# Kernel optimization log

Hardware: AMD Instinct MI355X
Metric: run time of the kernel (lower is better)

Reference implementation:

```python
import jax, jax.numpy as jnp
import numpy as np

L, D, F, T, V = 12, 1024, 4096, 128, 50257
RESCALE, TAU, EPS = 6, 2.0, 1e-5

# spikingjelly LIFNode spike: heaviside forward, ATan surrogate (alpha=2) backward
@jax.custom_vjp
def _heaviside(x):
    return (x >= 0.0).astype(x.dtype)

def _h_fwd(x):
    return (x >= 0.0).astype(x.dtype), x

def _h_bwd(x, g):
    return (g / (1.0 + (jnp.pi * x) ** 2),)

_heaviside.defvjp(_h_fwd, _h_bwd)


def _ln(x, w, b):
    m = jnp.mean(x)
    v = jnp.mean((x - m) ** 2)
    return (x - m) * jax.lax.rsqrt(v + EPS) * w + b


def _lif(v, x):
    # LIFNode(tau=2, v_threshold=1, v_reset=0, decay_input=True), single step
    v = v + (x - v) / TAU
    s = _heaviside(v - 1.0)
    return v * (1.0 - s), s  # hard reset, binary spike out


def _forward(tokens, emb, pos_emb, ln0_w, ln0_b, ln1_w, ln1_b, ln2_w, ln2_b,
             att_tmk, att_tmv, att_tmr, time_first, time_decay_raw,
             att_kw, att_vw, att_rw, att_ow, ffn_tmk, ffn_tmr,
             ffn_kw, ffn_vw, ffn_rw, lnout_w, lnout_b, head):
    td = -jnp.exp(time_decay_raw)  # load-time transform: time_decay = -exp(w)
    params = (ln1_w, ln1_b, ln2_w, ln2_b, att_tmk, att_tmv, att_tmr,
              time_first, td, att_kw, att_vw, att_rw, att_ow,
              ffn_tmk, ffn_tmr, ffn_kw, ffn_vw, ffn_rw)
    idx = jnp.arange(L)

    def layer_step(x, xs):
        i, p, st = xs
        (l1w, l1b, l2w, l2b, tmk, tmv, tmr, tf, tdec,
         kw, vw, rw, ow, ftmk, ftmr, fkw, fvw, frw) = p
        sx_ff, sx_att, aa, bb, pp, v1, v2 = st
        # ---- SA: time-mixing with exp-weighted state (aa, bb, pp) ----
        xa = _ln(x, l1w, l1b)
        xk = xa * tmk + sx_att * (1.0 - tmk)
        xv = xa * tmv + sx_att * (1.0 - tmv)
        xr = xa * tmr + sx_att * (1.0 - tmr)
        r = jax.nn.sigmoid(rw @ xr)
        k = kw @ xk
        v = vw @ xv
        ww = tf + k
        q = jnp.maximum(pp, ww)
        e1, e2 = jnp.exp(pp - q), jnp.exp(ww - q)
        a = e1 * aa + e2 * v
        b = e1 * bb + e2
        ww2 = pp + tdec
        q2 = jnp.maximum(ww2, k)
        e1, e2 = jnp.exp(ww2 - q2), jnp.exp(k - q2)
        aa_n = e1 * aa + e2 * v
        bb_n = e1 * bb + e2
        v1_n, sa_out = _lif(v1, ow @ (r * (a / b)))
        x = x + sa_out
        # ---- FF: channel mixing ----
        xf = _ln(x, l2w, l2b)
        fxk = xf * ftmk + sx_ff * (1.0 - ftmk)
        fxr = xf * ftmr + sx_ff * (1.0 - ftmr)
        fr = jax.nn.sigmoid(frw @ fxr)
        fk = jnp.square(jax.nn.relu(fkw @ fxk))
        v2_n, ff_out = _lif(v2, fr * (fvw @ fk))
        x = x + ff_out
        x = jnp.where((i + 1) % RESCALE == 0, x * 0.5, x)  # rwkv_rescale
        return x, (xf, xa, aa_n, bb_n, q2, v1_n, v2_n)

    def token_step(st, inp):
        tok, pe = inp
        x = emb[tok] + pe
        x = _ln(x, ln0_w, ln0_b)  # ln0 applied only at layer 0
        x, st_n = jax.lax.scan(layer_step, x, (idx, params, st))
        x = _ln(x, lnout_w, lnout_b)
        return st_n, head @ x

    zz = jnp.zeros((L, D), jnp.float32)
    st0 = (zz, zz, zz, zz, jnp.full((L, D), -1e30, jnp.float32), zz, zz)
    _, logits = jax.lax.scan(token_step, st0, (tokens, pos_emb))
    return logits  # [T, V]


def setup_inputs() -> dict:
    key = jax.random.key(0)
    ks = jax.random.split(key, 20)
    n = lambda k, s, sc: jax.random.normal(k, s, jnp.float32) * sc
    u = lambda k, s: jax.random.uniform(k, s, jnp.float32)
    return {
        "tokens": jax.random.randint(ks[0], (T,), 0, V, dtype=jnp.int32),
        "emb": n(ks[1], (V, D), 0.02),
        "pos_emb": n(ks[2], (T, D), 0.02),
        "ln0_w": jnp.ones((D,), jnp.float32), "ln0_b": jnp.zeros((D,), jnp.float32),
        "ln1_w": jnp.ones((L, D), jnp.float32), "ln1_b": jnp.zeros((L, D), jnp.float32),
        "ln2_w": jnp.ones((L, D), jnp.float32), "ln2_b": jnp.zeros((L, D), jnp.float32),
        "att_tmk": u(ks[3], (L, D)), "att_tmv": u(ks[4], (L, D)), "att_tmr": u(ks[5], (L, D)),
        "time_first": n(ks[6], (L, D), 0.5),
        "time_decay_raw": n(ks[7], (L, D), 0.5),
        "att_kw": n(ks[8], (L, D, D), 0.02), "att_vw": n(ks[9], (L, D, D), 0.02),
        "att_rw": n(ks[10], (L, D, D), 0.02), "att_ow": n(ks[11], (L, D, D), 0.02),
        "ffn_tmk": u(ks[12], (L, D)), "ffn_tmr": u(ks[13], (L, D)),
        "ffn_kw": n(ks[14], (L, F, D), 0.02), "ffn_vw": n(ks[15], (L, D, F), 0.02),
        "ffn_rw": n(ks[16], (L, D, D), 0.02),
        "lnout_w": jnp.ones((D,), jnp.float32), "lnout_b": jnp.zeros((D,), jnp.float32),
        "head": n(ks[17], (V, D), 0.02),
    }


def reference(tokens, emb, pos_emb, ln0_w, ln0_b, ln1_w, ln1_b, ln2_w, ln2_b,
              att_tmk, att_tmv, att_tmr, time_first, time_decay_raw,
              att_kw, att_vw, att_rw, att_ow, ffn_tmk, ffn_tmr,
              ffn_kw, ffn_vw, ffn_rw, lnout_w, lnout_b, head):
    return _forward(tokens, emb, pos_emb, ln0_w, ln0_b, ln1_w, ln1_b, ln2_w, ln2_b,
                    att_tmk, att_tmv, att_tmr, time_first, time_decay_raw,
                    att_kw, att_vw, att_rw, att_ow, ffn_tmk, ffn_tmr,
                    ffn_kw, ffn_vw, ffn_rw, lnout_w, lnout_b, head)
```

## Files before the change

### kernel.cpp

```cpp
#include <hip/hip_runtime.h>
#include <hip/hip_bf16.h>
#include <hip/hip_fp8.h>

#define LL   12
#define DD   1024
#define FF   4096
#define TTOK 128
#define VV   50257
#define NBLK 512
#define NTH  512
#define NGRP 12
#define GBLK 42
#define NHEAD (NBLK - NGRP * GBLK)
#define NSTEP (TTOK / 2 + NGRP)
#define WSC  256.0f
#define XSC  (1.0f / 256.0f)

__device__ __forceinline__ float cld(const float* p) {
    return __hip_atomic_load((float*)p, __ATOMIC_RELAXED, __HIP_MEMORY_SCOPE_AGENT);
}
__device__ __forceinline__ void cst(float* p, float v) {
    __hip_atomic_store(p, v, __ATOMIC_RELAXED, __HIP_MEMORY_SCOPE_AGENT);
}

__device__ __host__ __forceinline__ unsigned short f2bf(float f) {
    union { float f; unsigned u; } x; x.f = f;
    unsigned r = x.u + 0x7fffu + ((x.u >> 16) & 1u);
    return (unsigned short)(r >> 16);
}

__device__ __forceinline__ unsigned pack_bf2(float a, float b) {
    return (unsigned)f2bf(a) | ((unsigned)f2bf(b) << 16);
}

__device__ __forceinline__ void ld8(const float* p, float* o) {
    float4 a = ((const float4*)p)[0], b = ((const float4*)p)[1];
    o[0]=a.x; o[1]=a.y; o[2]=a.z; o[3]=a.w; o[4]=b.x; o[5]=b.y; o[6]=b.z; o[7]=b.w;
}

__device__ __forceinline__ void bf8unpack(uint4 u, float* o) {
    union { unsigned u; float f; } t;
    t.u = u.x << 16;         o[0] = t.f;
    t.u = u.x & 0xffff0000u; o[1] = t.f;
    t.u = u.y << 16;         o[2] = t.f;
    t.u = u.y & 0xffff0000u; o[3] = t.f;
    t.u = u.z << 16;         o[4] = t.f;
    t.u = u.z & 0xffff0000u; o[5] = t.f;
    t.u = u.w << 16;         o[6] = t.f;
    t.u = u.w & 0xffff0000u; o[7] = t.f;
}

__device__ __forceinline__ void xld8(const unsigned short* x, int chunk, float* o) {
    uint4 u = *reinterpret_cast<const uint4*>(x + (chunk << 3));
    bf8unpack(u, o);
}
__device__ __forceinline__ void xres(const unsigned short* xb, int lane, float* o) {
    xld8(xb, lane, o); xld8(xb, lane + 64, o + 8);
}

typedef __attribute__((ext_vector_type(2))) float f32x2_t;

__device__ __forceinline__ void fp8x4(unsigned v, float* o) {
#if __has_builtin(__builtin_amdgcn_cvt_pk_f32_fp8)
    f32x2_t a = __builtin_amdgcn_cvt_pk_f32_fp8(v, false);
    f32x2_t b = __builtin_amdgcn_cvt_pk_f32_fp8(v, true);
    o[0] = a[0]; o[1] = a[1]; o[2] = b[0]; o[3] = b[1];
#else
    #pragma unroll
    for (int i = 0; i < 4; ++i) {
        __hip_fp8_e4m3 t; t.__x = (__hip_fp8_storage_t)((v >> (8 * i)) & 0xffu);
        o[i] = (float)t;
    }
#endif
}

__device__ __forceinline__ unsigned enc_fp8x4(float4 f) {
#if __has_builtin(__builtin_amdgcn_cvt_pk_fp8_f32)
    int d = 0;
    d = __builtin_amdgcn_cvt_pk_fp8_f32(f.x, f.y, d, false);
    d = __builtin_amdgcn_cvt_pk_fp8_f32(f.z, f.w, d, true);
    return (unsigned)d;
#else
    __hip_fp8_e4m3 a(f.x), b(f.y), c(f.z), e(f.w);
    return (unsigned)a.__x | ((unsigned)b.__x << 8) |
           ((unsigned)c.__x << 16) | ((unsigned)e.__x << 24);
#endif
}

__device__ __forceinline__ float dot16u(uint4 w, const float* x) {
    float wf[4], s;
    fp8x4(w.x, wf); s  = wf[0]*x[0] +wf[1]*x[1] +wf[2]*x[2] +wf[3]*x[3];
    fp8x4(w.y, wf); s += wf[0]*x[4] +wf[1]*x[5] +wf[2]*x[6] +wf[3]*x[7];
    fp8x4(w.z, wf); s += wf[0]*x[8] +wf[1]*x[9] +wf[2]*x[10]+wf[3]*x[11];
    fp8x4(w.w, wf); s += wf[0]*x[12]+wf[1]*x[13]+wf[2]*x[14]+wf[3]*x[15];
    return s;
}
__device__ __forceinline__ float dot16f(const float* w, const float* x) {
    float s = 0.f;
    #pragma unroll
    for (int i = 0; i < 16; ++i) s += w[i] * x[i];
    return s;
}

template<bool F8> struct WSeg;
template<> struct WSeg<true>  { uint4 v; };
template<> struct WSeg<false> { float f[16]; };

__device__ __forceinline__ void wseg_load(WSeg<true>& d, const void* w, long row,
                                          int segs, int m, int lane) {
    d.v = *(const uint4*)((const unsigned char*)w + (((row * segs + m) << 10) + (lane << 4)));
}
__device__ __forceinline__ void wseg_load(WSeg<false>& d, const void* w, long row,
                                          int segs, int m, int lane) {
    const float* p = (const float*)w + ((long)(row * segs + m) << 10);
    ld8(p + (lane << 3), d.f);
    ld8(p + 512 + (lane << 3), d.f + 8);
}
__device__ __forceinline__ float wseg_dot(const WSeg<true>& d, const float* x) { return dot16u(d.v, x); }
__device__ __forceinline__ float wseg_dot(const WSeg<false>& d, const float* x) { return dot16f(d.f, x); }

__device__ __forceinline__ float wred(float s) {
    #pragma unroll
    for (int o = 32; o; o >>= 1) s += __shfl_xor(s, o, 64);
    return s;
}

__device__ __forceinline__ void bstats(const float* x, float* red, float& m, float& rs) {
    int tid = threadIdx.x;
    float a = x[tid], b = x[tid + 512];
    float s0 = a + b, s1 = a*a + b*b;
    #pragma unroll
    for (int o = 32; o; o >>= 1) { s0 += __shfl_xor(s0, o, 64); s1 += __shfl_xor(s1, o, 64); }
    if ((tid & 63) == 0) { red[(tid >> 6) * 2] = s0; red[(tid >> 6) * 2 + 1] = s1; }
    __syncthreads();
    float ms = 0.f, qs = 0.f;
    #pragma unroll
    for (int w = 0; w < 8; ++w) { ms += red[w * 2]; qs += red[w * 2 + 1]; }
    ms *= (1.f / 1024.f); qs *= (1.f / 1024.f);
    m = ms; rs = rsqrtf(qs - ms * ms + 1e-5f);
    __syncthreads();
}

__device__ __forceinline__ void grpbar(unsigned* bar, int grp, unsigned n, unsigned& sen) {
    __syncthreads();
    if (threadIdx.x == 0) {
        unsigned s = sen ^ 1u;
        unsigned* cnt = &bar[grp * 64];
        unsigned* sns = &bar[grp * 64 + 32];
        unsigned prev = __hip_atomic_fetch_add(cnt, 1u, __ATOMIC_RELAXED, __HIP_MEMORY_SCOPE_AGENT);
        if (prev == n - 1u) {
            __hip_atomic_store(cnt, 0u, __ATOMIC_RELAXED, __HIP_MEMORY_SCOPE_AGENT);
            asm volatile("s_waitcnt vmcnt(0)" ::: "memory");
            __hip_atomic_store(sns, s, __ATOMIC_RELAXED, __HIP_MEMORY_SCOPE_AGENT);
        } else {
            while (__hip_atomic_load(sns, __ATOMIC_RELAXED, __HIP_MEMORY_SCOPE_AGENT) != s)
                __builtin_amdgcn_s_sleep(1);
        }
    }
    sen ^= 1u;
    __syncthreads();
}

__device__ __forceinline__ void fpub(unsigned* f, unsigned v) {
    __hip_atomic_store(f, v, __ATOMIC_RELAXED, __HIP_MEMORY_SCOPE_AGENT);
}
__device__ __forceinline__ void fwait(unsigned* f, unsigned v) {
    while (__hip_atomic_load(f, __ATOMIC_RELAXED, __HIP_MEMORY_SCOPE_AGENT) < v)
        __builtin_amdgcn_s_sleep(1);
}

struct SP {
    const int* tok; const float* emb; const float* pos;
    const float *l0w, *l0b, *l1w, *l1b, *l2w, *l2b;
    const float *tmk, *tmv, *tmr, *tf, *tdr;
    const float *ftmk, *ftmr, *low, *lob;
    const void *kw, *vw, *rw, *ow, *fkw, *fvw, *frw;
    float *xg, *xmid, *rwkv, *fk, *td;
    float *aa, *bb, *pp, *sxa, *sxf, *v1, *v2;
    float* XbT;
    unsigned* bar;
};

template<bool F8>
__global__ __launch_bounds__(NTH, 4) void spike_wave(SP P) {
    const void* kw  = P.kw;
    const void* vw  = P.vw;
    const void* rw  = P.rw;
    const void* ow  = P.ow;
    const void* fkw = P.fkw;
    const void* fvw = P.fvw;
    const void* frw = P.frw;
    constexpr float XS = F8 ? XSC : 1.0f;

    __shared__ float xl[2][DD];
    __shared__ float xs1[DD];
    __shared__ __align__(16) unsigned short xkb[2][DD], xvb[2][DD], xrb[2][DD];
    __shared__ __align__(16) unsigned short fklb[2][FF];
    __shared__ float red[16];
    __shared__ float kres[2][32], vres[2][32], rres[2][32];
    __shared__ float frl2[2][32];

    const int tid  = threadIdx.x;
    const int b    = blockIdx.x;
    const int wid  = tid >> 6;
    const int lane = tid & 63;
    const bool isHead = (b >= NGRP * GBLK);
    const int grp = isHead ? NGRP : (b / GBLK);
    const int gi  = isHead ? (b - NGRP * GBLK) : (b % GBLK);
    const unsigned gn = isHead ? (unsigned)NHEAD : (unsigned)GBLK;
    int c_beg = 0, c_end = 0, r_beg = 0, r_end = 0;
    if (!isHead) {
        c_beg = (gi * DD) / GBLK; c_end = ((gi + 1) * DD) / GBLK;
        r_beg = (gi * FF) / GBLK; r_end = ((gi + 1) * FF) / GBLK;
    }
    const int nch = c_end - c_beg;
    const int  ld = (isHead ? 0 : grp) * DD;
    const long rw0 = (long)(grp * 2) * DD;
    const long fk0 = (long)(grp * 2) * FF;

    unsigned* done = P.bar + 1024;
    unsigned* rda  = P.bar + 2048;

    auto mat2 = [&](const void* wm, const unsigned short* xb, float* o0, float* o1) {
        float x0r[16], x1r[16];
        xres(xb, lane, x0r);
        xres(xb + DD, lane, x1r);
        for (int c0 = c_beg + (wid << 2); c0 < c_end; c0 += 32) {
            WSeg<F8> w[4];
            #pragma unroll
            for (int k = 0; k < 4; ++k) {
                int c = c0 + k;
                wseg_load(w[k], wm, (long)ld + (c < c_end ? c : c0), 1, 0, lane);
            }
            #pragma unroll
            for (int k = 0; k < 4; ++k) {
                float d0 = wred(wseg_dot(w[k], x0r));
                float d1 = wred(wseg_dot(w[k], x1r));
                if (lane == 0 && c0 + k < c_end) {
                    o0[c0 + k - c_beg] = d0; o1[c0 + k - c_beg] = d1;
                }
            }
        }
    };

    unsigned sen = 0;

    if (!isHead) {
        for (int c = c_beg + tid; c < c_end; c += NTH) {
            int si = ld + c;
            P.aa[si] = 0.f; P.bb[si] = 0.f; P.pp[si] = -1e30f;
            P.v1[si] = 0.f; P.v2[si] = 0.f;
            P.td[si] = -expf(P.tdr[si]);
            cst(&P.sxa[si], 0.f); cst(&P.sxf[si], 0.f);
        }
    }
    grpbar(P.bar, grp, gn, sen);

    #pragma unroll 1
    for (int s = 0; s < NSTEP; ++s) {
        const int t0 = 2 * (s - grp);
        const bool act = (t0 >= 0) && (t0 < TTOK);
        const unsigned wbuf = (unsigned)s & 1u, rbuf = wbuf ^ 1u;
        float* xgw = P.xg + (((size_t)wbuf * NGRP + (isHead ? 0 : grp)) * 2) * DD;
        const float* xgr = P.xg + (((size_t)rbuf * NGRP + (grp > 0 ? grp - 1 : 0)) * 2) * DD;

        if (act) {
            if (isHead) {
                if (tid == 0) fwait(&done[NGRP - 1], (unsigned)s);
                __syncthreads();
                xl[0][tid] = cld(&xgr[tid]);       xl[0][tid + 512] = cld(&xgr[tid + 512]);
                xl[1][tid] = cld(&xgr[DD + tid]);  xl[1][tid + 512] = cld(&xgr[DD + tid + 512]);
                __syncthreads();
                float m0, rs0, m1, rs1;
                bstats(xl[0], red, m0, rs0);
                bstats(xl[1], red, m1, rs1);
                for (int cc = (gi << 7) + tid; cc < ((gi + 1) << 7); cc += NTH) {
                    P.XbT[(size_t)cc * TTOK + t0]     = (xl[0][cc] - m0) * rs0 * P.low[cc] + P.lob[cc];
                    P.XbT[(size_t)cc * TTOK + t0 + 1] = (xl[1][cc] - m1) * rs1 * P.low[cc] + P.lob[cc];
                }
            } else {
                if (grp == 0) {
                    int tk0 = P.tok[t0], tk1 = P.tok[t0 + 1];
                    #pragma unroll
                    for (int tk = 0; tk < 2; ++tk) {
                        size_t eb = (size_t)(tk ? tk1 : tk0) * DD;
                        size_t pb = (size_t)(t0 + tk) * DD;
                        float e0 = P.emb[eb + tid]       + P.pos[pb + tid];
                        float e1 = P.emb[eb + tid + 512] + P.pos[pb + tid + 512];
                        xl[tk][tid] = e0; xl[tk][tid + 512] = e1;
                        __syncthreads();
                        float m, rs; bstats(xl[tk], red, m, rs);
                        xl[tk][tid]       = (e0 - m) * rs * P.l0w[tid]       + P.l0b[tid];
                        xl[tk][tid + 512] = (e1 - m) * rs * P.l0w[tid + 512] + P.l0b[tid + 512];
                        __syncthreads();
                    }
                } else {
                    if (tid == 0) fwait(&done[grp - 1], (unsigned)s);
                    __syncthreads();
                    xl[0][tid] = cld(&xgr[tid]);       xl[0][tid + 512] = cld(&xgr[tid + 512]);
                    xl[1][tid] = cld(&xgr[DD + tid]);  xl[1][tid + 512] = cld(&xgr[DD + tid + 512]);
                    __syncthreads();
                }
                float m0, rs0, m1, rs1;
                bstats(xl[0], red, m0, rs0);
                bstats(xl[1], red, m1, rs1);
                {
                    int i2 = tid << 1;
                    float2 w2 = *(const float2*)&P.l1w[ld + i2];
                    float2 b2 = *(const float2*)&P.l1b[ld + i2];
                    float2 uk = *(const float2*)&P.tmk[ld + i2];
                    float2 uv = *(const float2*)&P.tmv[ld + i2];
                    float2 ur = *(const float2*)&P.tmr[ld + i2];
                    float a0 = (xl[0][i2]     - m0) * rs0 * w2.x + b2.x;
                    float a1 = (xl[0][i2 + 1] - m0) * rs0 * w2.y + b2.y;
                    float sx0 = cld(&P.sxa[ld + i2]), sx1 = cld(&P.sxa[ld + i2 + 1]);
                    ((unsigned*)xkb[0])[tid] = pack_bf2((a0*uk.x + sx0*(1.f-uk.x))*XS, (a1*uk.y + sx1*(1.f-uk.y))*XS);
                    ((unsigned*)xvb[0])[tid] = pack_bf2((a0*uv.x + sx0*(1.f-uv.x))*XS, (a1*uv.y + sx1*(1.f-uv.y))*XS);
                    ((unsigned*)xrb[0])[tid] = pack_bf2((a0*ur.x + sx0*(1.f-ur.x))*XS, (a1*ur.y + sx1*(1.f-ur.y))*XS);
                    float c0v = (xl[1][i2]     - m1) * rs1 * w2.x + b2.x;
                    float c1v = (xl[1][i2 + 1] - m1) * rs1 * w2.y + b2.y;
                    xs1[i2] = c0v; xs1[i2 + 1] = c1v;
                    ((unsigned*)xkb[1])[tid] = pack_bf2((c0v*uk.x + a0*(1.f-uk.x))*XS, (c1v*uk.y + a1*(1.f-uk.y))*XS);
                    ((unsigned*)xvb[1])[tid] = pack_bf2((c0v*uv.x + a0*(1.f-uv.x))*XS, (c1v*uv.y + a1*(1.f-uv.y))*XS);
                    ((unsigned*)xrb[1])[tid] = pack_bf2((c0v*ur.x + a0*(1.f-ur.x))*XS, (c1v*ur.y + a1*(1.f-ur.y))*XS);
                }
                __syncthreads();
                mat2(kw, xkb[0], kres[0], kres[1]);
                mat2(vw, xvb[0], vres[0], vres[1]);
                mat2(rw, xrb[0], rres[0], rres[1]);
                __syncthreads();
                if (tid < nch) {
                    int c = c_beg + tid, si = ld + c;
                    float aa = P.aa[si], bb = P.bb[si], pp = P.pp[si];
                    float tf = P.tf[si], tdv = P.td[si];
                    #pragma unroll
                    for (int tk = 0; tk < 2; ++tk) {
                        float kk = kres[tk][tid], vv = vres[tk][tid], rr = rres[tk][tid];
                        float ww = tf + kk;
                        float q  = fmaxf(pp, ww);
                        float e1 = expf(pp - q), e2 = expf(ww - q);
                        float an = e1 * aa + e2 * vv, bn = e1 * bb + e2;
                        float ww2 = pp + tdv;
                        float q2  = fmaxf(ww2, kk);
                        float e1b = expf(ww2 - q2), e2b = expf(kk - q2);
                        aa = e1b * aa + e2b * vv;
                        bb = e1b * bb + e2b;
                        pp = q2;
                        float sg = 1.f / (1.f + expf(-rr));
                        cst(&P.rwkv[rw0 + tk * DD + c], sg * (an / bn));
                    }
                    P.aa[si] = aa; P.bb[si] = bb; P.pp[si] = pp;
                }
            }
        }
        grpbar(P.bar, grp, gn, sen);
        if (gi == 0 && tid == 0) fpub(&rda[grp], (unsigned)(s + 1));

        if (act && !isHead) {
            for (int c = c_beg + tid; c < c_end; c += NTH)
                cst(&P.sxa[ld + c], xs1[c]);
            {
                int i2 = tid << 1;
                ((unsigned*)xvb[0])[tid] = pack_bf2(cld(&P.rwkv[rw0 + i2]) * XS,
                                                    cld(&P.rwkv[rw0 + i2 + 1]) * XS);
                ((unsigned*)xvb[1])[tid] = pack_bf2(cld(&P.rwkv[rw0 + DD + i2]) * XS,
                                                    cld(&P.rwkv[rw0 + DD + i2 + 1]) * XS);
            }
            __syncthreads();
            mat2(ow, xvb[0], kres[0], kres[1]);
            __syncthreads();
            if (tid < nch) {
                int c = c_beg + tid, si = ld + c;
                float v1v = P.v1[si];
                float vn = v1v + (kres[0][tid] - v1v) * 0.5f;
                float sp0 = (vn >= 1.f) ? 1.f : 0.f;  v1v = vn * (1.f - sp0);
                vn = v1v + (kres[1][tid] - v1v) * 0.5f;
                float sp1 = (vn >= 1.f) ? 1.f : 0.f;  v1v = vn * (1.f - sp1);
                P.v1[si] = v1v;
                cst(&P.xmid[rw0 + c],      xl[0][c] + sp0);
                cst(&P.xmid[rw0 + DD + c], xl[1][c] + sp1);
            }
        }
        grpbar(P.bar, grp, gn, sen);

        if (act && !isHead) {
            xl[0][tid] = cld(&P.xmid[rw0 + tid]);       xl[0][tid + 512] = cld(&P.xmid[rw0 + tid + 512]);
            xl[1][tid] = cld(&P.xmid[rw0 + DD + tid]);  xl[1][tid + 512] = cld(&P.xmid[rw0 + DD + tid + 512]);
            __syncthreads();
            float m0, rs0, m1, rs1;
            bstats(xl[0], red, m0, rs0);
            bstats(xl[1], red, m1, rs1);
            {
                int i2 = tid << 1;
                float2 w2 = *(const float2*)&P.l2w[ld + i2];
                float2 b2 = *(const float2*)&P.l2b[ld + i2];
                float2 uk = *(const float2*)&P.ftmk[ld + i2];
                float2 ur = *(const float2*)&P.ftmr[ld + i2];
                float f0 = (xl[0][i2]     - m0) * rs0 * w2.x + b2.x;
                float f1 = (xl[0][i2 + 1] - m0) * rs0 * w2.y + b2.y;
                float sx0 = cld(&P.sxf[ld + i2]), sx1 = cld(&P.sxf[ld + i2 + 1]);
                ((unsigned*)xkb[0])[tid] = pack_bf2((f0*uk.x + sx0*(1.f-uk.x))*XS, (f1*uk.y + sx1*(1.f-uk.y))*XS);
                ((unsigned*)xrb[0])[tid] = pack_bf2((f0*ur.x + sx0*(1.f-ur.x))*XS, (f1*ur.y + sx1*(1.f-ur.y))*XS);
                float g0 = (xl[1][i2]     - m1) * rs1 * w2.x + b2.x;
                float g1 = (xl[1][i2 + 1] - m1) * rs1 * w2.y + b2.y;
                xs1[i2] = g0; xs1[i2 + 1] = g1;
                ((unsigned*)xkb[1])[tid] = pack_bf2((g0*uk.x + f0*(1.f-uk.x))*XS, (g1*uk.y + f1*(1.f-uk.y))*XS);
                ((unsigned*)xrb[1])[tid] = pack_bf2((g0*ur.x + f0*(1.f-ur.x))*XS, (g1*ur.y + f1*(1.f-ur.y))*XS);
            }
            __syncthreads();
            {
                float x0r[16], x1r[16];
                xres(xkb[0], lane, x0r); xres(xkb[1], lane, x1r);
                for (int r0 = r_beg + (wid << 2); r0 < r_end; r0 += 32) {
                    WSeg<F8> w[4];
                    #pragma unroll
                    for (int k = 0; k < 4; ++k) {
                        int ri = r0 + k;
                        wseg_load(w[k], fkw, (long)grp * FF + (ri < r_end ? ri : r0), 1, 0, lane);
                    }
                    #pragma unroll
                    for (int k = 0; k < 4; ++k) {
                        if (r0 + k < r_end) {
                            float d0 = wred(wseg_dot(w[k], x0r));
                            float d1 = wred(wseg_dot(w[k], x1r));
                            if (lane == 0) {
                                float u0 = fmaxf(d0, 0.f); cst(&P.fk[fk0 + r0 + k], u0 * u0);
                                float u1 = fmaxf(d1, 0.f); cst(&P.fk[fk0 + FF + r0 + k], u1 * u1);
                            }
                        }
                    }
                }
            }
            mat2(frw, xrb[0], frl2[0], frl2[1]);
        }
        grpbar(P.bar, grp, gn, sen);

        if (act && !isHead) {
            if (tid == 0 && s > 0) fwait(&rda[grp + 1], (unsigned)s);
            __syncthreads();
            for (int c = c_beg + tid; c < c_end; c += NTH)
                cst(&P.sxf[ld + c], xs1[c]);
            {
                float la[4], lb[4], lc[4], ldv[4];
                #pragma unroll
                for (int j = 0; j < 4; ++j) {
                    int e = (tid << 1) + (j << 10);
                    la[j]  = cld(&P.fk[fk0 + e]);      lb[j]  = cld(&P.fk[fk0 + e + 1]);
                    lc[j]  = cld(&P.fk[fk0 + FF + e]); ldv[j] = cld(&P.fk[fk0 + FF + e + 1]);
                }
                #pragma unroll
                for (int j = 0; j < 4; ++j) {
                    ((unsigned*)fklb[0])[tid + (j << 9)] = pack_bf2(la[j] * XS, lb[j] * XS);
                    ((unsigned*)fklb[1])[tid + (j << 9)] = pack_bf2(lc[j] * XS, ldv[j] * XS);
                }
            }
            __syncthreads();
            {
                for (int c0 = c_beg + (wid << 2); c0 < c_end; c0 += 32) {
                    float acc0[4], acc1[4];
                    #pragma unroll
                    for (int k = 0; k < 4; ++k) { acc0[k] = 0.f; acc1[k] = 0.f; }
                    #pragma unroll 1
                    for (int m = 0; m < 4; ++m) {
                        WSeg<F8> w[4];
                        #pragma unroll
                        for (int k = 0; k < 4; ++k) {
                            int c = c0 + k;
                            wseg_load(w[k], fvw, (long)ld + (c < c_end ? c : c0), 4, m, lane);
                        }
                        float xf0[16], xf1[16];
                        xld8(fklb[0], (m << 7) + lane, xf0);
                        xld8(fklb[0], (m << 7) + 64 + lane, xf0 + 8);
                        xld8(fklb[1], (m << 7) + lane, xf1);
                        xld8(fklb[1], (m << 7) + 64 + lane, xf1 + 8);
                        #pragma unroll
                        for (int k = 0; k < 4; ++k) {
                            acc0[k] += wseg_dot(w[k], xf0);
                            acc1[k] += wseg_dot(w[k], xf1);
                        }
                    }
                    #pragma unroll
                    for (int k = 0; k < 4; ++k) {
                        float f0 = wred(acc0[k]), f1 = wred(acc1[k]);
                        if (lane == 0 && c0 + k < c_end) {
                            kres[0][c0 + k - c_beg] = f0;
                            kres[1][c0 + k - c_beg] = f1;
                        }
                    }
                }
            }
            __syncthreads();
            if (tid < nch) {
                int c = c_beg + tid, si = ld + c;
                float v2v = P.v2[si];
                float fr0 = 1.f / (1.f + expf(-frl2[0][tid]));
                float fr1 = 1.f / (1.f + expf(-frl2[1][tid]));
                float hh = fr0 * kres[0][tid];
                float vn = v2v + (hh - v2v) * 0.5f;
                float sp0 = (vn >= 1.f) ? 1.f : 0.f;  v2v = vn * (1.f - sp0);
                hh = fr1 * kres[1][tid];
                vn = v2v + (hh - v2v) * 0.5f;
                float sp1 = (vn >= 1.f) ? 1.f : 0.f;  v2v = vn * (1.f - sp1);
                P.v2[si] = v2v;
                float xn0 = xl[0][c] + sp0, xn1 = xl[1][c] + sp1;
                if (((grp + 1) % 6) == 0) { xn0 *= 0.5f; xn1 *= 0.5f; }
                cst(&xgw[c], xn0);
                cst(&xgw[DD + c], xn1);
            }
        }
        grpbar(P.bar, grp, gn, sen);
        if (gi == 0 && tid == 0) fpub(&done[grp], (unsigned)(s + 1));
    }
}

__global__ __launch_bounds__(256) void head_simple(const float* __restrict__ head,
                                                   const float* __restrict__ XbT,
                                                   float* __restrict__ out) {
    int wv   = __builtin_amdgcn_readfirstlane(threadIdx.x >> 6);
    int lane = threadIdx.x & 63;
    int v0   = (blockIdx.x * 4 + wv) * 8;
    if (v0 >= VV) return;
    const float* hp[8];
    #pragma unroll
    for (int r = 0; r < 8; ++r) {
        int v = v0 + r; if (v >= VV) v = VV - 1;
        hp[r] = head + (size_t)v * DD;
    }
    float a0[8], a1[8];
    #pragma unroll
    for (int r = 0; r < 8; ++r) { a0[r] = 0.f; a1[r] = 0.f; }
    #pragma unroll 4
    for (int k = 0; k < DD; ++k) {
        float2 x2 = *(const float2*)(XbT + (size_t)k * TTOK + lane * 2);
        #pragma unroll
        for (int r = 0; r < 8; ++r) {
            float hv = hp[r][k];
            a0[r] += hv * x2.x;
            a1[r] += hv * x2.y;
        }
    }
    int t0 = lane * 2, t1 = t0 + 1;
    #pragma unroll
    for (int r = 0; r < 8; ++r) {
        int v = v0 + r;
        if (v < VV) {
            out[(size_t)t0 * VV + v] = a0[r];
            out[(size_t)t1 * VV + v] = a1[r];
        }
    }
}

__global__ void cvt_fp8(const float* __restrict__ s, unsigned char* __restrict__ d, long n) {
    long p4 = ((long)blockIdx.x * blockDim.x + threadIdx.x) * 4;
    long st = (long)gridDim.x * blockDim.x * 4;
    for (; p4 < n; p4 += st) {
        long seg = p4 >> 10;
        int  q   = (int)(p4 & 1023);
        int  u   = q >> 4, rem = q & 15, half = rem >> 3, j0 = rem & 7;
        long e = (seg << 10) + ((long)half << 9) + (u << 3) + j0;
        float4 f = *(const float4*)(s + e);
        f.x *= WSC; f.y *= WSC; f.z *= WSC; f.w *= WSC;
        *(unsigned*)(d + p4) = enc_fp8x4(f);
    }
}

extern "C" void kernel_launch(void* const* d_in, const int* in_sizes, int n_in,
                              void* d_out, int out_size, void* d_ws, size_t ws_size,
                              hipStream_t stream) {
    (void)in_sizes; (void)n_in; (void)out_size;
    char* base = (char*)d_ws;
    size_t off = 0;
    auto take = [&](size_t bytes) -> void* {
        void* p = base + off;
        off = (off + bytes + 255) & ~(size_t)255;
        return p;
    };
    unsigned* bar = (unsigned*)take(16384);
    float* xg   = (float*)take((size_t)2 * NGRP * 2 * DD * 4);
    float* xmid = (float*)take((size_t)NGRP * 2 * DD * 4);
    float* rwkv = (float*)take((size_t)NGRP * 2 * DD * 4);
    float* fk   = (float*)take((size_t)NGRP * 2 * FF * 4);
    float* td   = (float*)take(LL * DD * 4);
    float* aa   = (float*)take(LL * DD * 4);
    float* bb   = (float*)take(LL * DD * 4);
    float* pp   = (float*)take(LL * DD * 4);
    float* sxa  = (float*)take(LL * DD * 4);
    float* sxf  = (float*)take(LL * DD * 4);
    float* v1   = (float*)take(LL * DD * 4);
    float* v2   = (float*)take(LL * DD * 4);
    float* XbT  = (float*)take((size_t)DD * TTOK * 4);
    size_t wDD = (size_t)LL * DD * DD;
    size_t wFD = (size_t)LL * FF * DD;
    unsigned char* kwb  = (unsigned char*)take(wDD);
    unsigned char* vwb  = (unsigned char*)take(wDD);
    unsigned char* rwb  = (unsigned char*)take(wDD);
    unsigned char* owb  = (unsigned char*)take(wDD);
    unsigned char* frwb = (unsigned char*)take(wDD);
    unsigned char* fkwb = (unsigned char*)take(wFD);
    unsigned char* fvwb = (unsigned char*)take(wFD);
    bool usef8 = (ws_size >= off);

    hipMemsetAsync(bar, 0, 16384, stream);

    SP P;
    P.tok = (const int*)d_in[0];
    P.emb = (const float*)d_in[1];
    P.pos = (const float*)d_in[2];
    P.l0w = (const float*)d_in[3];  P.l0b = (const float*)d_in[4];
    P.l1w = (const float*)d_in[5];  P.l1b = (const float*)d_in[6];
    P.l2w = (const float*)d_in[7];  P.l2b = (const float*)d_in[8];
    P.tmk = (const float*)d_in[9];  P.tmv = (const float*)d_in[10]; P.tmr = (const float*)d_in[11];
    P.tf  = (const float*)d_in[12]; P.tdr = (const float*)d_in[13];
    P.ftmk = (const float*)d_in[18]; P.ftmr = (const float*)d_in[19];
    P.low = (const float*)d_in[23]; P.lob = (const float*)d_in[24];
    P.xg = xg; P.xmid = xmid; P.rwkv = rwkv; P.fk = fk; P.td = td;
    P.aa = aa; P.bb = bb; P.pp = pp; P.sxa = sxa; P.sxf = sxf; P.v1 = v1; P.v2 = v2;
    P.XbT = XbT; P.bar = bar;

    if (usef8) {
        struct CV { const float* s; unsigned char* d; size_t n; } cv[7] = {
            {(const float*)d_in[14], kwb,  wDD}, {(const float*)d_in[15], vwb,  wDD},
            {(const float*)d_in[16], rwb,  wDD}, {(const float*)d_in[17], owb,  wDD},
            {(const float*)d_in[22], frwb, wDD},
            {(const float*)d_in[20], fkwb, wFD}, {(const float*)d_in[21], fvwb, wFD},
        };
        for (int i = 0; i < 7; ++i)
            cvt_fp8<<<dim3(2048), dim3(256), 0, stream>>>(cv[i].s, cv[i].d, (long)cv[i].n);
        P.kw = kwb; P.vw = vwb; P.rw = rwb; P.ow = owb; P.fkw = fkwb; P.fvw = fvwb; P.frw = frwb;
        spike_wave<true><<<dim3(NBLK), dim3(NTH), 0, stream>>>(P);
    } else {
        P.kw = d_in[14]; P.vw = d_in[15]; P.rw = d_in[16]; P.ow = d_in[17];
        P.fkw = d_in[20]; P.fvw = d_in[21]; P.frw = d_in[22];
        spike_wave<false><<<dim3(NBLK), dim3(NTH), 0, stream>>>(P);
    }
    int nwave = (VV + 7) / 8;
    int nblk  = (nwave + 3) / 4;
    head_simple<<<dim3(nblk), dim3(256), 0, stream>>>((const float*)d_in[25], XbT,
                                                      (float*)d_out);
}
```

Baseline: 5.316 ms.

## Process four tokens per wave step and use hierarchical group barriers

Raises tokens per pipeline step from 2 to 4, so each weight segment loaded from memory is reused across four token vectors in every matvec. This halves the number of wavefront steps and the group barriers and global handoffs tied to them. The group barrier also becomes a two-level tree: sub-counters of up to 8 blocks feed one top counter, whose winner releases a per-subgroup sense flag, which cuts contention on a single atomic. The cost is more shared memory and registers per block, which can lower occupancy. Pipeline fill and drain across the 12 layer groups also grows longer relative to the total number of steps.

```diff
diff --git a/kernel.cpp b/kernel.cpp
--- a/kernel.cpp
+++ b/kernel.cpp
@@ -12,7 +12,8 @@
 #define NGRP 12
 #define GBLK 42
 #define NHEAD (NBLK - NGRP * GBLK)
-#define NSTEP (TTOK / 2 + NGRP)
+#define TPS  4
+#define NSTEP (TTOK / TPS + NGRP)
 #define WSC  256.0f
 #define XSC  (1.0f / 256.0f)
 
@@ -141,19 +142,31 @@
     __syncthreads();
 }
 
-__device__ __forceinline__ void grpbar(unsigned* bar, int grp, unsigned n, unsigned& sen) {
+__device__ __forceinline__ void grpbar(unsigned* bar, int grp, int gi, unsigned gn, unsigned& sen) {
     __syncthreads();
     if (threadIdx.x == 0) {
         unsigned s = sen ^ 1u;
-        unsigned* cnt = &bar[grp * 64];
-        unsigned* sns = &bar[grp * 64 + 32];
-        unsigned prev = __hip_atomic_fetch_add(cnt, 1u, __ATOMIC_RELAXED, __HIP_MEMORY_SCOPE_AGENT);
-        if (prev == n - 1u) {
-            __hip_atomic_store(cnt, 0u, __ATOMIC_RELAXED, __HIP_MEMORY_SCOPE_AGENT);
+        unsigned* B = bar + grp * 256;
+        int sub = gi >> 3;
+        unsigned nsub = (gn + 7u) >> 3;
+        unsigned rem  = gn - (unsigned)(sub << 3);
+        unsigned subn = rem < 8u ? rem : 8u;
+        unsigned p = __hip_atomic_fetch_add(&B[sub * 8], 1u, __ATOMIC_RELAXED, __HIP_MEMORY_SCOPE_AGENT);
+        bool flipped = false;
+        if (p == subn - 1u) {
+            __hip_atomic_store(&B[sub * 8], 0u, __ATOMIC_RELAXED, __HIP_MEMORY_SCOPE_AGENT);
             asm volatile("s_waitcnt vmcnt(0)" ::: "memory");
-            __hip_atomic_store(sns, s, __ATOMIC_RELAXED, __HIP_MEMORY_SCOPE_AGENT);
-        } else {
-            while (__hip_atomic_load(sns, __ATOMIC_RELAXED, __HIP_MEMORY_SCOPE_AGENT) != s)
+            unsigned q = __hip_atomic_fetch_add(&B[64], 1u, __ATOMIC_RELAXED, __HIP_MEMORY_SCOPE_AGENT);
+            if (q == nsub - 1u) {
+                __hip_atomic_store(&B[64], 0u, __ATOMIC_RELAXED, __HIP_MEMORY_SCOPE_AGENT);
+                asm volatile("s_waitcnt vmcnt(0)" ::: "memory");
+                for (unsigned j = 0; j < nsub; ++j)
+                    __hip_atomic_store(&B[128 + j * 8], s, __ATOMIC_RELAXED, __HIP_MEMORY_SCOPE_AGENT);
+                flipped = true;
+            }
+        }
+        if (!flipped) {
+            while (__hip_atomic_load(&B[128 + sub * 8], __ATOMIC_RELAXED, __HIP_MEMORY_SCOPE_AGENT) != s)
                 __builtin_amdgcn_s_sleep(1);
         }
     }
@@ -192,13 +205,12 @@
     const void* frw = P.frw;
     constexpr float XS = F8 ? XSC : 1.0f;
 
-    __shared__ float xl[2][DD];
-    __shared__ float xs1[DD];
-    __shared__ __align__(16) unsigned short xkb[2][DD], xvb[2][DD], xrb[2][DD];
-    __shared__ __align__(16) unsigned short fklb[2][FF];
+    __shared__ float xl[TPS][DD];
+    __shared__ __align__(16) unsigned short xkb[TPS][DD], xvb[TPS][DD], xrb[TPS][DD];
+    __shared__ __align__(16) unsigned short fklb[TPS][FF];
     __shared__ float red[16];
-    __shared__ float kres[2][32], vres[2][32], rres[2][32];
-    __shared__ float frl2[2][32];
+    __shared__ float kres[TPS][32], vres[TPS][32], rres[TPS][32];
+    __shared__ float frl2[TPS][32];
 
     const int tid  = threadIdx.x;
     const int b    = blockIdx.x;
@@ -215,16 +227,13 @@
     }
     const int nch = c_end - c_beg;
     const int  ld = (isHead ? 0 : grp) * DD;
-    const long rw0 = (long)(grp * 2) * DD;
-    const long fk0 = (long)(grp * 2) * FF;
-
-    unsigned* done = P.bar + 1024;
-    unsigned* rda  = P.bar + 2048;
-
-    auto mat2 = [&](const void* wm, const unsigned short* xb, float* o0, float* o1) {
-        float x0r[16], x1r[16];
-        xres(xb, lane, x0r);
-        xres(xb + DD, lane, x1r);
+    const long rw0 = (long)(grp * TPS) * DD;
+    const long fk0 = (long)(grp * TPS) * FF;
+
+    unsigned* done = P.bar + 8192;
+    unsigned* rda  = P.bar + 8192 + 256;
+
+    auto mat4 = [&](const void* wm, const unsigned short* xb, float (*o)[32]) {
         for (int c0 = c_beg + (wid << 2); c0 < c_end; c0 += 32) {
             WSeg<F8> w[4];
             #pragma unroll
@@ -233,17 +242,31 @@
                 wseg_load(w[k], wm, (long)ld + (c < c_end ? c : c0), 1, 0, lane);
             }
             #pragma unroll
-            for (int k = 0; k < 4; ++k) {
-                float d0 = wred(wseg_dot(w[k], x0r));
-                float d1 = wred(wseg_dot(w[k], x1r));
-                if (lane == 0 && c0 + k < c_end) {
-                    o0[c0 + k - c_beg] = d0; o1[c0 + k - c_beg] = d1;
+            for (int tp = 0; tp < TPS / 2; ++tp) {
+                float d[2][4];
+                #pragma unroll
+                for (int th = 0; th < 2; ++th) {
+                    float xr[16];
+                    xres(xb + (tp * 2 + th) * DD, lane, xr);
+                    #pragma unroll
+                    for (int k = 0; k < 4; ++k) d[th][k] = wseg_dot(w[k], xr);
+                }
+                #pragma unroll
+                for (int th = 0; th < 2; ++th) {
+                    #pragma unroll
+                    for (int k = 0; k < 4; ++k) {
+                        float dv = wred(d[th][k]);
+                        if (lane == 0 && c0 + k < c_end)
+                            o[tp * 2 + th][c0 + k - c_beg] = dv;
+                    }
                 }
             }
         }
     };
 
     unsigned sen = 0;
+    float xa3_0 = 0.f, xa3_1 = 0.f;
+    float xf3_0 = 0.f, xf3_1 = 0.f;
 
     if (!isHead) {
         for (int c = c_beg + tid; c < c_end; c += NTH) {
@@ -254,36 +277,39 @@
             cst(&P.sxa[si], 0.f); cst(&P.sxf[si], 0.f);
         }
     }
-    grpbar(P.bar, grp, gn, sen);
+    grpbar(P.bar, grp, gi, gn, sen);
 
     #pragma unroll 1
     for (int s = 0; s < NSTEP; ++s) {
-        const int t0 = 2 * (s - grp);
+        const int t0 = TPS * (s - grp);
         const bool act = (t0 >= 0) && (t0 < TTOK);
         const unsigned wbuf = (unsigned)s & 1u, rbuf = wbuf ^ 1u;
-        float* xgw = P.xg + (((size_t)wbuf * NGRP + (isHead ? 0 : grp)) * 2) * DD;
-        const float* xgr = P.xg + (((size_t)rbuf * NGRP + (grp > 0 ? grp - 1 : 0)) * 2) * DD;
+        float* xgw = P.xg + (((size_t)wbuf * NGRP + (isHead ? 0 : grp)) * TPS) * DD;
+        const float* xgr = P.xg + (((size_t)rbuf * NGRP + (grp > 0 ? grp - 1 : 0)) * TPS) * DD;
 
         if (act) {
             if (isHead) {
                 if (tid == 0) fwait(&done[NGRP - 1], (unsigned)s);
                 __syncthreads();
-                xl[0][tid] = cld(&xgr[tid]);       xl[0][tid + 512] = cld(&xgr[tid + 512]);
-                xl[1][tid] = cld(&xgr[DD + tid]);  xl[1][tid + 512] = cld(&xgr[DD + tid + 512]);
+                #pragma unroll
+                for (int tk = 0; tk < TPS; ++tk) {
+                    xl[tk][tid]       = cld(&xgr[tk * DD + tid]);
+                    xl[tk][tid + 512] = cld(&xgr[tk * DD + tid + 512]);
+                }
                 __syncthreads();
-                float m0, rs0, m1, rs1;
-                bstats(xl[0], red, m0, rs0);
-                bstats(xl[1], red, m1, rs1);
-                for (int cc = (gi << 7) + tid; cc < ((gi + 1) << 7); cc += NTH) {
-                    P.XbT[(size_t)cc * TTOK + t0]     = (xl[0][cc] - m0) * rs0 * P.low[cc] + P.lob[cc];
-                    P.XbT[(size_t)cc * TTOK + t0 + 1] = (xl[1][cc] - m1) * rs1 * P.low[cc] + P.lob[cc];
+                #pragma unroll 1
+                for (int tk = 0; tk < TPS; ++tk) {
+                    float m, rs; bstats(xl[tk], red, m, rs);
+                    for (int cc = (gi << 7) + tid; cc < ((gi + 1) << 7); cc += NTH)
+                        P.XbT[(size_t)cc * TTOK + t0 + tk] =
+                            (xl[tk][cc] - m) * rs * P.low[cc] + P.lob[cc];
                 }
             } else {
                 if (grp == 0) {
-                    int tk0 = P.tok[t0], tk1 = P.tok[t0 + 1];
-                    #pragma unroll
-                    for (int tk = 0; tk < 2; ++tk) {
-                        size_t eb = (size_t)(tk ? tk1 : tk0) * DD;
+                    #pragma unroll 1
+                    for (int tk = 0; tk < TPS; ++tk) {
+                        int tkn = P.tok[t0 + tk];
+                        size_t eb = (size_t)tkn * DD;
                         size_t pb = (size_t)(t0 + tk) * DD;
                         float e0 = P.emb[eb + tid]       + P.pos[pb + tid];
                         float e1 = P.emb[eb + tid + 512] + P.pos[pb + tid + 512];
@@ -297,13 +323,16 @@
                 } else {
                     if (tid == 0) fwait(&done[grp - 1], (unsigned)s);
                     __syncthreads();
-                    xl[0][tid] = cld(&xgr[tid]);       xl[0][tid + 512] = cld(&xgr[tid + 512]);
-                    xl[1][tid] = cld(&xgr[DD + tid]);  xl[1][tid + 512] = cld(&xgr[DD + tid + 512]);
+                    #pragma unroll
+                    for (int tk = 0; tk < TPS; ++tk) {
+                        xl[tk][tid]       = cld(&xgr[tk * DD + tid]);
+                        xl[tk][tid + 512] = cld(&xgr[tk * DD + tid + 512]);
+                    }
                     __syncthreads();
                 }
-                float m0, rs0, m1, rs1;
-                bstats(xl[0], red, m0, rs0);
-                bstats(xl[1], red, m1, rs1);
+                float mm[TPS], rr[TPS];
+                #pragma unroll 1
+                for (int tk = 0; tk < TPS; ++tk) bstats(xl[tk], red, mm[tk], rr[tk]);
                 {
                     int i2 = tid << 1;
                     float2 w2 = *(const float2*)&P.l1w[ld + i2];
@@ -311,31 +340,30 @@
                     float2 uk = *(const float2*)&P.tmk[ld + i2];
                     float2 uv = *(const float2*)&P.tmv[ld + i2];
                     float2 ur = *(const float2*)&P.tmr[ld + i2];
-                    float a0 = (xl[0][i2]     - m0) * rs0 * w2.x + b2.x;
-                    float a1 = (xl[0][i2 + 1] - m0) * rs0 * w2.y + b2.y;
                     float sx0 = cld(&P.sxa[ld + i2]), sx1 = cld(&P.sxa[ld + i2 + 1]);
-                    ((unsigned*)xkb[0])[tid] = pack_bf2((a0*uk.x + sx0*(1.f-uk.x))*XS, (a1*uk.y + sx1*(1.f-uk.y))*XS);
-                    ((unsigned*)xvb[0])[tid] = pack_bf2((a0*uv.x + sx0*(1.f-uv.x))*XS, (a1*uv.y + sx1*(1.f-uv.y))*XS);
-                    ((unsigned*)xrb[0])[tid] = pack_bf2((a0*ur.x + sx0*(1.f-ur.x))*XS, (a1*ur.y + sx1*(1.f-ur.y))*XS);
-                    float c0v = (xl[1][i2]     - m1) * rs1 * w2.x + b2.x;
-                    float c1v = (xl[1][i2 + 1] - m1) * rs1 * w2.y + b2.y;
-                    xs1[i2] = c0v; xs1[i2 + 1] = c1v;
-                    ((unsigned*)xkb[1])[tid] = pack_bf2((c0v*uk.x + a0*(1.f-uk.x))*XS, (c1v*uk.y + a1*(1.f-uk.y))*XS);
-                    ((unsigned*)xvb[1])[tid] = pack_bf2((c0v*uv.x + a0*(1.f-uv.x))*XS, (c1v*uv.y + a1*(1.f-uv.y))*XS);
-                    ((unsigned*)xrb[1])[tid] = pack_bf2((c0v*ur.x + a0*(1.f-ur.x))*XS, (c1v*ur.y + a1*(1.f-ur.y))*XS);
+                    #pragma unroll
+                    for (int tk = 0; tk < TPS; ++tk) {
+                        float a0 = (xl[tk][i2]     - mm[tk]) * rr[tk] * w2.x + b2.x;
+                        float a1 = (xl[tk][i2 + 1] - mm[tk]) * rr[tk] * w2.y + b2.y;
+                        ((unsigned*)xkb[tk])[tid] = pack_bf2((a0*uk.x + sx0*(1.f-uk.x))*XS, (a1*uk.y + sx1*(1.f-uk.y))*XS);
+                        ((unsigned*)xvb[tk])[tid] = pack_bf2((a0*uv.x + sx0*(1.f-uv.x))*XS, (a1*uv.y + sx1*(1.f-uv.y))*XS);
+                        ((unsigned*)xrb[tk])[tid] = pack_bf2((a0*ur.x + sx0*(1.f-ur.x))*XS, (a1*ur.y + sx1*(1.f-ur.y))*XS);
+                        sx0 = a0; sx1 = a1;
+                    }
+                    xa3_0 = sx0; xa3_1 = sx1;
                 }
                 __syncthreads();
-                mat2(kw, xkb[0], kres[0], kres[1]);
-                mat2(vw, xvb[0], vres[0], vres[1]);
-                mat2(rw, xrb[0], rres[0], rres[1]);
+                mat4(kw, xkb[0], kres);
+                mat4(vw, xvb[0], vres);
+                mat4(rw, xrb[0], rres);
                 __syncthreads();
                 if (tid < nch) {
                     int c = c_beg + tid, si = ld + c;
                     float aa = P.aa[si], bb = P.bb[si], pp = P.pp[si];
                     float tf = P.tf[si], tdv = P.td[si];
                     #pragma unroll
-                    for (int tk = 0; tk < 2; ++tk) {
-                        float kk = kres[tk][tid], vv = vres[tk][tid], rr = rres[tk][tid];
+                    for (int tk = 0; tk < TPS; ++tk) {
+                        float kk = kres[tk][tid], vv = vres[tk][tid], rv = rres[tk][tid];
                         float ww = tf + kk;
                         float q  = fmaxf(pp, ww);
                         float e1 = expf(pp - q), e2 = expf(ww - q);
@@ -346,71 +374,77 @@
                         aa = e1b * aa + e2b * vv;
                         bb = e1b * bb + e2b;
                         pp = q2;
-                        float sg = 1.f / (1.f + expf(-rr));
+                        float sg = 1.f / (1.f + expf(-rv));
                         cst(&P.rwkv[rw0 + tk * DD + c], sg * (an / bn));
                     }
                     P.aa[si] = aa; P.bb[si] = bb; P.pp[si] = pp;
                 }
             }
         }
-        grpbar(P.bar, grp, gn, sen);
+        grpbar(P.bar, grp, gi, gn, sen);
         if (gi == 0 && tid == 0) fpub(&rda[grp], (unsigned)(s + 1));
 
         if (act && !isHead) {
-            for (int c = c_beg + tid; c < c_end; c += NTH)
-                cst(&P.sxa[ld + c], xs1[c]);
+            {
+                int e0 = tid << 1;
+                if (e0 >= c_beg && e0 < c_end)         cst(&P.sxa[ld + e0], xa3_0);
+                if (e0 + 1 >= c_beg && e0 + 1 < c_end) cst(&P.sxa[ld + e0 + 1], xa3_1);
+            }
             {
                 int i2 = tid << 1;
-                ((unsigned*)xvb[0])[tid] = pack_bf2(cld(&P.rwkv[rw0 + i2]) * XS,
-                                                    cld(&P.rwkv[rw0 + i2 + 1]) * XS);
-                ((unsigned*)xvb[1])[tid] = pack_bf2(cld(&P.rwkv[rw0 + DD + i2]) * XS,
-                                                    cld(&P.rwkv[rw0 + DD + i2 + 1]) * XS);
+                #pragma unroll
+                for (int tk = 0; tk < TPS; ++tk)
+                    ((unsigned*)xvb[tk])[tid] =
+                        pack_bf2(cld(&P.rwkv[rw0 + tk * DD + i2]) * XS,
+                                 cld(&P.rwkv[rw0 + tk * DD + i2 + 1]) * XS);
             }
             __syncthreads();
-            mat2(ow, xvb[0], kres[0], kres[1]);
+            mat4(ow, xvb[0], kres);
             __syncthreads();
             if (tid < nch) {
                 int c = c_beg + tid, si = ld + c;
                 float v1v = P.v1[si];
-                float vn = v1v + (kres[0][tid] - v1v) * 0.5f;
-                float sp0 = (vn >= 1.f) ? 1.f : 0.f;  v1v = vn * (1.f - sp0);
-                vn = v1v + (kres[1][tid] - v1v) * 0.5f;
-                float sp1 = (vn >= 1.f) ? 1.f : 0.f;  v1v = vn * (1.f - sp1);
+                #pragma unroll
+                for (int tk = 0; tk < TPS; ++tk) {
+                    float vn = v1v + (kres[tk][tid] - v1v) * 0.5f;
+                    float sp = (vn >= 1.f) ? 1.f : 0.f;
+                    v1v = vn * (1.f - sp);
+                    cst(&P.xmid[rw0 + tk * DD + c], xl[tk][c] + sp);
+                }
                 P.v1[si] = v1v;
-                cst(&P.xmid[rw0 + c],      xl[0][c] + sp0);
-                cst(&P.xmid[rw0 + DD + c], xl[1][c] + sp1);
-            }
-        }
-        grpbar(P.bar, grp, gn, sen);
+            }
+        }
+        grpbar(P.bar, grp, gi, gn, sen);
 
         if (act && !isHead) {
-            xl[0][tid] = cld(&P.xmid[rw0 + tid]);       xl[0][tid + 512] = cld(&P.xmid[rw0 + tid + 512]);
-            xl[1][tid] = cld(&P.xmid[rw0 + DD + tid]);  xl[1][tid + 512] = cld(&P.xmid[rw0 + DD + tid + 512]);
+            #pragma unroll
+            for (int tk = 0; tk < TPS; ++tk) {
+                xl[tk][tid]       = cld(&P.xmid[rw0 + tk * DD + tid]);
+                xl[tk][tid + 512] = cld(&P.xmid[rw0 + tk * DD + tid + 512]);
+            }
             __syncthreads();
-            float m0, rs0, m1, rs1;
-            bstats(xl[0], red, m0, rs0);
-            bstats(xl[1], red, m1, rs1);
+            float mm[TPS], rr[TPS];
+            #pragma unroll 1
+            for (int tk = 0; tk < TPS; ++tk) bstats(xl[tk], red, mm[tk], rr[tk]);
             {
                 int i2 = tid << 1;
                 float2 w2 = *(const float2*)&P.l2w[ld + i2];
                 float2 b2 = *(const float2*)&P.l2b[ld + i2];
                 float2 uk = *(const float2*)&P.ftmk[ld + i2];
                 float2 ur = *(const float2*)&P.ftmr[ld + i2];
-                float f0 = (xl[0][i2]     - m0) * rs0 * w2.x + b2.x;
-                float f1 = (xl[0][i2 + 1] - m0) * rs0 * w2.y + b2.y;
                 float sx0 = cld(&P.sxf[ld + i2]), sx1 = cld(&P.sxf[ld + i2 + 1]);
-                ((unsigned*)xkb[0])[tid] = pack_bf2((f0*uk.x + sx0*(1.f-uk.x))*XS, (f1*uk.y + sx1*(1.f-uk.y))*XS);
-                ((unsigned*)xrb[0])[tid] = pack_bf2((f0*ur.x + sx0*(1.f-ur.x))*XS, (f1*ur.y + sx1*(1.f-ur.y))*XS);
-                float g0 = (xl[1][i2]     - m1) * rs1 * w2.x + b2.x;
-                float g1 = (xl[1][i2 + 1] - m1) * rs1 * w2.y + b2.y;
-                xs1[i2] = g0; xs1[i2 + 1] = g1;
-                ((unsigned*)xkb[1])[tid] = pack_bf2((g0*uk.x + f0*(1.f-uk.x))*XS, (g1*uk.y + f1*(1.f-uk.y))*XS);
-                ((unsigned*)xrb[1])[tid] = pack_bf2((g0*ur.x + f0*(1.f-ur.x))*XS, (g1*ur.y + f1*(1.f-ur.y))*XS);
+                #pragma unroll
+                for (int tk = 0; tk < TPS; ++tk) {
+                    float f0 = (xl[tk][i2]     - mm[tk]) * rr[tk] * w2.x + b2.x;
+                    float f1 = (xl[tk][i2 + 1] - mm[tk]) * rr[tk] * w2.y + b2.y;
+                    ((unsigned*)xkb[tk])[tid] = pack_bf2((f0*uk.x + sx0*(1.f-uk.x))*XS, (f1*uk.y + sx1*(1.f-uk.y))*XS);
+                    ((unsigned*)xrb[tk])[tid] = pack_bf2((f0*ur.x + sx0*(1.f-ur.x))*XS, (f1*ur.y + sx1*(1.f-ur.y))*XS);
+                    sx0 = f0; sx1 = f1;
+                }
+                xf3_0 = sx0; xf3_1 = sx1;
             }
             __syncthreads();
             {
-                float x0r[16], x1r[16];
-                xres(xkb[0], lane, x0r); xres(xkb[1], lane, x1r);
                 for (int r0 = r_beg + (wid << 2); r0 < r_end; r0 += 32) {
                     WSeg<F8> w[4];
                     #pragma unroll
@@ -419,47 +453,62 @@
                         wseg_load(w[k], fkw, (long)grp * FF + (ri < r_end ? ri : r0), 1, 0, lane);
                     }
                     #pragma unroll
-                    for (int k = 0; k < 4; ++k) {
-                        if (r0 + k < r_end) {
-                            float d0 = wred(wseg_dot(w[k], x0r));
-                            float d1 = wred(wseg_dot(w[k], x1r));
-                            if (lane == 0) {
-                                float u0 = fmaxf(d0, 0.f); cst(&P.fk[fk0 + r0 + k], u0 * u0);
-                                float u1 = fmaxf(d1, 0.f); cst(&P.fk[fk0 + FF + r0 + k], u1 * u1);
+                    for (int tp = 0; tp < TPS / 2; ++tp) {
+                        float d[2][4];
+                        #pragma unroll
+                        for (int th = 0; th < 2; ++th) {
+                            float xr[16];
+                            xres(xkb[tp * 2 + th], lane, xr);
+                            #pragma unroll
+                            for (int k = 0; k < 4; ++k) d[th][k] = wseg_dot(w[k], xr);
+                        }
+                        #pragma unroll
+                        for (int th = 0; th < 2; ++th) {
+                            #pragma unroll
+                            for (int k = 0; k < 4; ++k) {
+                                float dv = wred(d[th][k]);
+                                if (lane == 0 && r0 + k < r_end) {
+                                    float u = fmaxf(dv, 0.f);
+                                    cst(&P.fk[fk0 + (tp * 2 + th) * FF + r0 + k], u * u);
+                                }
                             }
                         }
                     }
                 }
             }
-            mat2(frw, xrb[0], frl2[0], frl2[1]);
-        }
-        grpbar(P.bar, grp, gn, sen);
+            mat4(frw, xrb[0], frl2);
+        }
+        grpbar(P.bar, grp, gi, gn, sen);
 
         if (act && !isHead) {
             if (tid == 0 && s > 0) fwait(&rda[grp + 1], (unsigned)s);
             __syncthreads();
-            for (int c = c_beg + tid; c < c_end; c += NTH)
-                cst(&P.sxf[ld + c], xs1[c]);
             {
-                float la[4], lb[4], lc[4], ldv[4];
+                int e0 = tid << 1;
+                if (e0 >= c_beg && e0 < c_end)         cst(&P.sxf[ld + e0], xf3_0);
+                if (e0 + 1 >= c_beg && e0 + 1 < c_end) cst(&P.sxf[ld + e0 + 1], xf3_1);
+            }
+            #pragma unroll 1
+            for (int tk = 0; tk < TPS; ++tk) {
+                float la[4], lb[4];
                 #pragma unroll
                 for (int j = 0; j < 4; ++j) {
                     int e = (tid << 1) + (j << 10);
-                    la[j]  = cld(&P.fk[fk0 + e]);      lb[j]  = cld(&P.fk[fk0 + e + 1]);
-                    lc[j]  = cld(&P.fk[fk0 + FF + e]); ldv[j] = cld(&P.fk[fk0 + FF + e + 1]);
-                }
-                #pragma unroll
-                for (int j = 0; j < 4; ++j) {
-                    ((unsigned*)fklb[0])[tid + (j << 9)] = pack_bf2(la[j] * XS, lb[j] * XS);
-                    ((unsigned*)fklb[1])[tid + (j << 9)] = pack_bf2(lc[j] * XS, ldv[j] * XS);
-                }
+                    la[j] = cld(&P.fk[fk0 + tk * FF + e]);
+                    lb[j] = cld(&P.fk[fk0 + tk * FF + e + 1]);
+                }
+                #pragma unroll
+                for (int j = 0; j < 4; ++j)
+                    ((unsigned*)fklb[tk])[tid + (j << 9)] = pack_bf2(la[j] * XS, lb[j] * XS);
             }
             __syncthreads();
             {
                 for (int c0 = c_beg + (wid << 2); c0 < c_end; c0 += 32) {
-                    float acc0[4], acc1[4];
-                    #pragma unroll
-                    for (int k = 0; k < 4; ++k) { acc0[k] = 0.f; acc1[k] = 0.f; }
+                    float acc[TPS][4];
+                    #pragma unroll
+                    for (int tk = 0; tk < TPS; ++tk)
+                        #pragma unroll
+                        for (int k = 0; k < 4; ++k) acc[tk][k] = 0.f;
                     #pragma unroll 1
                     for (int m = 0; m < 4; ++m) {
                         WSeg<F8> w[4];
@@ -468,47 +517,44 @@
                             int c = c0 + k;
                             wseg_load(w[k], fvw, (long)ld + (c < c_end ? c : c0), 4, m, lane);
                         }
-                        float xf0[16], xf1[16];
-                        xld8(fklb[0], (m << 7) + lane, xf0);
-                        xld8(fklb[0], (m << 7) + 64 + lane, xf0 + 8);
-                        xld8(fklb[1], (m << 7) + lane, xf1);
-                        xld8(fklb[1], (m << 7) + 64 + lane, xf1 + 8);
+                        #pragma unroll
+                        for (int tk = 0; tk < TPS; ++tk) {
+                            float xf[16];
+                            xld8(fklb[tk], (m << 7) + lane, xf);
+                            xld8(fklb[tk], (m << 7) + 64 + lane, xf + 8);
+                            #pragma unroll
+                            for (int k = 0; k < 4; ++k) acc[tk][k] += wseg_dot(w[k], xf);
+                        }
+                    }
+                    #pragma unroll
+                    for (int tk = 0; tk < TPS; ++tk)
                         #pragma unroll
                         for (int k = 0; k < 4; ++k) {
-                            acc0[k] += wseg_dot(w[k], xf0);
-                            acc1[k] += wseg_dot(w[k], xf1);
+                            float fv = wred(acc[tk][k]);
+                            if (lane == 0 && c0 + k < c_end)
+                                kres[tk][c0 + k - c_beg] = fv;
                         }
-                    }
-                    #pragma unroll
-                    for (int k = 0; k < 4; ++k) {
-                        float f0 = wred(acc0[k]), f1 = wred(acc1[k]);
-                        if (lane == 0 && c0 + k < c_end) {
-                            kres[0][c0 + k - c_beg] = f0;
-                            kres[1][c0 + k - c_beg] = f1;
-                        }
-                    }
                 }
             }
             __syncthreads();
             if (tid < nch) {
                 int c = c_beg + tid, si = ld + c;
                 float v2v = P.v2[si];
-                float fr0 = 1.f / (1.f + expf(-frl2[0][tid]));
-                float fr1 = 1.f / (1.f + expf(-frl2[1][tid]));
-                float hh = fr0 * kres[0][tid];
-                float vn = v2v + (hh - v2v) * 0.5f;
-                float sp0 = (vn >= 1.f) ? 1.f : 0.f;  v2v = vn * (1.f - sp0);
-                hh = fr1 * kres[1][tid];
-                vn = v2v + (hh - v2v) * 0.5f;
-                float sp1 = (vn >= 1.f) ? 1.f : 0.f;  v2v = vn * (1.f - sp1);
+                #pragma unroll
+                for (int tk = 0; tk < TPS; ++tk) {
+                    float fr = 1.f / (1.f + expf(-frl2[tk][tid]));
+                    float hh = fr * kres[tk][tid];
+                    float vn = v2v + (hh - v2v) * 0.5f;
+                    float sp = (vn >= 1.f) ? 1.f : 0.f;
+                    v2v = vn * (1.f - sp);
+                    float xn = xl[tk][c] + sp;
+                    if (((grp + 1) % 6) == 0) xn *= 0.5f;
+                    cst(&xgw[tk * DD + c], xn);
+                }
                 P.v2[si] = v2v;
-                float xn0 = xl[0][c] + sp0, xn1 = xl[1][c] + sp1;
-                if (((grp + 1) % 6) == 0) { xn0 *= 0.5f; xn1 *= 0.5f; }
-                cst(&xgw[c], xn0);
-                cst(&xgw[DD + c], xn1);
-            }
-        }
-        grpbar(P.bar, grp, gn, sen);
+            }
+        }
+        grpbar(P.bar, grp, gi, gn, sen);
         if (gi == 0 && tid == 0) fpub(&done[grp], (unsigned)(s + 1));
     }
 }
@@ -575,11 +621,11 @@
         off = (off + bytes + 255) & ~(size_t)255;
         return p;
     };
-    unsigned* bar = (unsigned*)take(16384);
-    float* xg   = (float*)take((size_t)2 * NGRP * 2 * DD * 4);
-    float* xmid = (float*)take((size_t)NGRP * 2 * DD * 4);
-    float* rwkv = (float*)take((size_t)NGRP * 2 * DD * 4);
-    float* fk   = (float*)take((size_t)NGRP * 2 * FF * 4);
+    unsigned* bar = (unsigned*)take(65536);
+    float* xg   = (float*)take((size_t)2 * NGRP * TPS * DD * 4);
+    float* xmid = (float*)take((size_t)NGRP * TPS * DD * 4);
+    float* rwkv = (float*)take((size_t)NGRP * TPS * DD * 4);
+    float* fk   = (float*)take((size_t)NGRP * TPS * FF * 4);
     float* td   = (float*)take(LL * DD * 4);
     float* aa   = (float*)take(LL * DD * 4);
     float* bb   = (float*)take(LL * DD * 4);
@@ -600,7 +646,7 @@
     unsigned char* fvwb = (unsigned char*)take(wFD);
     bool usef8 = (ws_size >= off);
 
-    hipMemsetAsync(bar, 0, 16384, stream);
+    hipMemsetAsync(bar, 0, 65536, stream);
 
     SP P;
     P.tok = (const int*)d_in[0];
```

After: 8.680 ms. 63.3% more time.
